# Kernel tuning notes

Hardware: AMD Instinct MI355X
Metric: run time of the kernel (lower is better)

## Reference

```python
import jax, jax.numpy as jnp
import numpy as np

B, S, H = 16, 512, 768
T, HD = 9, 64  # num_entity_types, head_size
MASK_VAL = 1e12


def setup_inputs() -> dict:
    key = jax.random.key(0)
    k1, k2 = jax.random.split(key)
    hidden_states = jax.random.normal(k1, (B, S, H), dtype=jnp.float32)
    attention_mask = jnp.ones((B, S), dtype=jnp.int32)
    W_dense = jax.random.normal(k2, (H, T * HD * 2), dtype=jnp.float32) * (H ** -0.5)
    b_dense = jnp.zeros((T * HD * 2,), dtype=jnp.float32)
    return {"hidden_states": hidden_states, "attention_mask": attention_mask,
            "W_dense": W_dense, "b_dense": b_dense}


def _rope_rotate(x, cos_pos, sin_pos):
    # x: [B, S, T, HD]; rotate interleaved pairs
    x2 = jnp.stack([-x[..., 1::2], x[..., ::2]], axis=-1).reshape(x.shape)
    return x * cos_pos + x2 * sin_pos


def reference(hidden_states, attention_mask, W_dense, b_dense):
    b, s, _ = hidden_states.shape
    out = hidden_states @ W_dense + b_dense              # [B,S,T*HD*2]
    out = out.reshape(b, s, T, HD, 2)
    qw, kw = out[..., 0], out[..., 1]                    # [B,S,T,HD]

    # sinusoidal RoPE angles
    pos = jnp.arange(s, dtype=jnp.float32)               # [S]
    inv_freq = jnp.power(10000.0, -2.0 * jnp.arange(HD // 2, dtype=jnp.float32) / HD)
    ang = pos[:, None] * inv_freq[None, :]               # [S, HD/2]
    cos_pos = jnp.repeat(jnp.cos(ang), 2, axis=-1)[None, :, None, :]  # [1,S,1,HD]
    sin_pos = jnp.repeat(jnp.sin(ang), 2, axis=-1)[None, :, None, :]

    qw = _rope_rotate(qw, cos_pos, sin_pos)
    kw = _rope_rotate(kw, cos_pos, sin_pos)

    # biaffine scores: [B,T,S,S]
    logits = jnp.einsum('bmtd,bntd->btmn', qw, kw) / (HD ** 0.5)

    am = attention_mask.astype(logits.dtype)
    pad_mask = (am[:, :, None] * am[:, None, :])[:, None, :, :]  # [B,1,S,S]
    logits = logits - (1.0 - pad_mask) * MASK_VAL

    triu = jnp.triu(jnp.ones((s, s), dtype=logits.dtype), k=0)
    logits = logits - (1.0 - triu) * MASK_VAL
    return logits
```

## Files before the change

kernel.cpp:

```cpp
#include <hip/hip_runtime.h>

#define B_  16
#define S_  512
#define H_  768
#define T_  9
#define HD_ 64
#define N1  (T_*HD_*2)
#define M1  (B_*S_)
#define NT1 (H_/32)

typedef __attribute__((ext_vector_type(8))) short bf16x8;
typedef __attribute__((ext_vector_type(4))) float f32x4;

#define GLB(p) ((const __attribute__((address_space(1))) void*)(p))
#define LDSP(p) ((__attribute__((address_space(3))) void*)(p))

__device__ inline unsigned short f2bf(float f){
  union { float f; unsigned u; } v; v.f = f;
  unsigned r = v.u + 0x7fffu + ((v.u >> 16) & 1u);
  return (unsigned short)(r >> 16);
}

__global__ __launch_bounds__(256) void prep_all(
    const float* __restrict__ hs, short* __restrict__ Abf,
    const float* __restrict__ W, short* __restrict__ Wt,
    float2* __restrict__ tab)
{
  __shared__ float tile[32][33];
  const int bx = blockIdx.x, tid = threadIdx.x;
  if(bx < 3072){
    int i = bx*2048 + tid*8;
    float4 a0 = *(const float4*)(hs + i);
    float4 a1 = *(const float4*)(hs + i + 4);
    bf16x8 r;
    r[0]=f2bf(a0.x); r[1]=f2bf(a0.y); r[2]=f2bf(a0.z); r[3]=f2bf(a0.w);
    r[4]=f2bf(a1.x); r[5]=f2bf(a1.y); r[6]=f2bf(a1.z); r[7]=f2bf(a1.w);
    *(bf16x8*)(Abf + i) = r;
  } else if(bx < 3936){
    int idx = bx - 3072;
    int n0 = (idx % 36)*32, k0 = (idx / 36)*32;
    int tx = tid & 31, ty = tid >> 5;
    #pragma unroll
    for(int r = 0; r < 32; r += 8)
      tile[ty + r][tx] = W[(size_t)(k0 + ty + r)*N1 + n0 + tx];
    __syncthreads();
    #pragma unroll
    for(int r = 0; r < 32; r += 8)
      Wt[(size_t)(n0 + ty + r)*H_ + k0 + tx] = (short)f2bf(tile[tx][ty + r]);
  } else {
    int i = (bx - 3936)*256 + tid;
    int s = i >> 5, p = i & 31;
    float inv = powf(10000.f, -2.f*(float)p/64.f);
    float a = (float)s * inv;
    tab[i] = make_float2(cosf(a), sinf(a));
  }
}

__global__ __launch_bounds__(256, 3) void gemm1_rope(
    const short* __restrict__ Abf, const short* __restrict__ Wt,
    const float* __restrict__ bias, const float2* __restrict__ tab,
    short* __restrict__ Qr, short* __restrict__ Kr)
{
  __shared__ short As[3][4096];
  __shared__ short Bs[3][4096];
  const int tid  = threadIdx.x;
  const int lane = tid & 63, w = tid >> 6;
  const int lr = lane & 15, h = lane >> 4;
  const int lk = h * 8;
  const int wm = (w >> 1) * 64, wn = (w & 1) * 64;
  const int m0 = blockIdx.x * 128;
  const int n0 = blockIdx.y * 128;

  const short* aS = Abf + (size_t)(m0 + (tid >> 2)) * H_ + (tid & 3) * 8;
  const short* bS = Wt  + (size_t)(n0 + (tid >> 2)) * H_ + (tid & 3) * 8;
  const int dOff = tid * 8;

#define STAGE(buf, k0) do{ \
    __builtin_amdgcn_global_load_lds(GLB(aS + (k0)),         LDSP(&As[buf][dOff]),        16, 0, 0); \
    __builtin_amdgcn_global_load_lds(GLB(aS + 64*H_ + (k0)), LDSP(&As[buf][dOff + 2048]), 16, 0, 0); \
    __builtin_amdgcn_global_load_lds(GLB(bS + (k0)),         LDSP(&Bs[buf][dOff]),        16, 0, 0); \
    __builtin_amdgcn_global_load_lds(GLB(bS + 64*H_ + (k0)), LDSP(&Bs[buf][dOff + 2048]), 16, 0, 0); \
  }while(0)

  f32x4 acc[4][4] = {};

  STAGE(0, 0);
  STAGE(1, 32);
  asm volatile("s_waitcnt vmcnt(4)\n\ts_barrier" ::: "memory");

  int cur = 0;
  for(int it = 0; it < NT1; ++it){
    if(it + 2 < NT1){
      const int nb = (cur + 2 >= 3) ? cur - 1 : cur + 2;
      STAGE(nb, (it + 2) * 32);
    }

    bf16x8 aF[4], bF[4];
    #pragma unroll
    for(int i = 0; i < 4; ++i) aF[i] = *(const bf16x8*)(&As[cur][(wm + i*16 + lr)*32 + lk]);
    #pragma unroll
    for(int j = 0; j < 4; ++j) bF[j] = *(const bf16x8*)(&Bs[cur][(wn + j*16 + lr)*32 + lk]);
    #pragma unroll
    for(int i = 0; i < 4; ++i)
      #pragma unroll
      for(int j = 0; j < 4; ++j)
        acc[i][j] = __builtin_amdgcn_mfma_f32_16x16x32_bf16(bF[j], aF[i], acc[i][j], 0, 0, 0);

    if(it + 3 < NT1)       asm volatile("s_waitcnt vmcnt(4)\n\ts_barrier" ::: "memory");
    else if(it + 2 < NT1)  asm volatile("s_waitcnt vmcnt(4)\n\ts_barrier" ::: "memory");
    else if(it + 1 < NT1)  asm volatile("s_waitcnt vmcnt(0)\n\ts_barrier" ::: "memory");
    cur = (cur + 1 >= 3) ? 0 : cur + 1;
  }

  const int t = blockIdx.y;
  #pragma unroll
  for(int i = 0; i < 4; ++i){
    int m  = m0 + wm + i*16 + lr;
    int bi = m >> 9, sp = m & 511;
    size_t rowoff = ((size_t)(bi*T_ + t)*S_ + sp)*HD_;
    #pragma unroll
    for(int j = 0; j < 4; ++j){
      int nq  = n0 + wn + j*16 + (h << 2);
      int hd0 = (nq >> 1) & 63;
      int p   = (nq >> 2) & 31;
      float4 bv = *(const float4*)(bias + nq);
      float2 cs = tab[sp*32 + p];
      float q0 = acc[i][j][0] + bv.x;
      float k0v= acc[i][j][1] + bv.y;
      float q1 = acc[i][j][2] + bv.z;
      float k1v= acc[i][j][3] + bv.w;
      float rq0 = q0*cs.x - q1*cs.y, rq1 = q1*cs.x + q0*cs.y;
      float rk0 = k0v*cs.x - k1v*cs.y, rk1 = k1v*cs.x + k0v*cs.y;
      unsigned uq = (unsigned)f2bf(rq0) | ((unsigned)f2bf(rq1) << 16);
      unsigned uk = (unsigned)f2bf(rk0) | ((unsigned)f2bf(rk1) << 16);
      *(unsigned*)(Qr + rowoff + hd0) = uq;
      *(unsigned*)(Kr + rowoff + hd0) = uk;
    }
  }
#undef STAGE
}

__global__ __launch_bounds__(256) void gemm2_mask(
    const short* __restrict__ Qr, const short* __restrict__ Kr,
    const int* __restrict__ am, float* __restrict__ out)
{
  const int lane = threadIdx.x & 63;
  const int w    = threadIdx.x >> 6;
  const int wg   = ((blockIdx.x & 7) * 288) + (blockIdx.x >> 3);
  const int bt   = wg >> 4;
  const int tile = wg & 15;
  const int mt   = tile >> 2, nt = tile & 3;
  const int b    = bt / T_;
  const int n0   = nt * 128 + (w & 1) * 64;
  const int m0   = mt * 128 + (w >> 1) * 64;
  const int lr   = lane & 15;
  const int lk   = (lane >> 4) * 8;
  const int* amb = am + b * S_;

  if(mt > nt){
    #pragma unroll
    for(int i = 0; i < 4; ++i){
      int m = m0 + i*16 + lr;
      float amm = (float)amb[m];
      float* orow = out + ((size_t)bt*S_ + m)*S_;
      #pragma unroll
      for(int j = 0; j < 4; ++j){
        int nq = n0 + j*16 + ((lane >> 4) << 2);
        int4 a4 = *(const int4*)(amb + nq);
        float4 r;
        r.x = -(1.f - amm*(float)a4.x)*1e12f - 1e12f;
        r.y = -(1.f - amm*(float)a4.y)*1e12f - 1e12f;
        r.z = -(1.f - amm*(float)a4.z)*1e12f - 1e12f;
        r.w = -(1.f - amm*(float)a4.w)*1e12f - 1e12f;
        *(float4*)(orow + nq) = r;
      }
    }
    return;
  }

  const short* Q = Qr + (size_t)bt * S_ * HD_;
  const short* K = Kr + (size_t)bt * S_ * HD_;
  f32x4 acc[4][4] = {};

  #pragma unroll
  for(int ks = 0; ks < HD_; ks += 32){
    bf16x8 aF[4], bF[4];
    #pragma unroll
    for(int i = 0; i < 4; ++i) aF[i] = *(const bf16x8*)(Q + (size_t)(m0 + i*16 + lr)*HD_ + ks + lk);
    #pragma unroll
    for(int j = 0; j < 4; ++j) bF[j] = *(const bf16x8*)(K + (size_t)(n0 + j*16 + lr)*HD_ + ks + lk);
    #pragma unroll
    for(int i = 0; i < 4; ++i)
      #pragma unroll
      for(int j = 0; j < 4; ++j)
        acc[i][j] = __builtin_amdgcn_mfma_f32_16x16x32_bf16(bF[j], aF[i], acc[i][j], 0, 0, 0);
  }

  const bool diag = (mt == nt);
  #pragma unroll
  for(int i = 0; i < 4; ++i){
    int m = m0 + i*16 + lr;
    float amm = (float)amb[m];
    float* orow = out + ((size_t)bt*S_ + m)*S_;
    #pragma unroll
    for(int j = 0; j < 4; ++j){
      int nq = n0 + j*16 + ((lane >> 4) << 2);
      int4 a4 = *(const int4*)(amb + nq);
      float4 r;
      r.x = acc[i][j][0]*0.125f - (1.f - amm*(float)a4.x)*1e12f;
      r.y = acc[i][j][1]*0.125f - (1.f - amm*(float)a4.y)*1e12f;
      r.z = acc[i][j][2]*0.125f - (1.f - amm*(float)a4.z)*1e12f;
      r.w = acc[i][j][3]*0.125f - (1.f - amm*(float)a4.w)*1e12f;
      if(diag){
        if((nq+0) < m) r.x -= 1e12f;
        if((nq+1) < m) r.y -= 1e12f;
        if((nq+2) < m) r.z -= 1e12f;
        if((nq+3) < m) r.w -= 1e12f;
      }
      *(float4*)(orow + nq) = r;
    }
  }
}

extern "C" void kernel_launch(void* const* d_in, const int* in_sizes, int n_in,
                              void* d_out, int out_size, void* d_ws, size_t ws_size,
                              hipStream_t stream)
{
  const float* hs    = (const float*)d_in[0];
  const int*   amask = (const int*)  d_in[1];
  const float* W     = (const float*)d_in[2];
  const float* bias  = (const float*)d_in[3];
  float* out = (float*)d_out;

  char* ws = (char*)d_ws;
  short*  Wt  = (short*) (ws);
  float2* tab = (float2*)(ws + 1769472);
  short*  Qr  = (short*) (ws + 1900544);
  short*  Kr  = (short*) (ws + 11337728);
  short*  Abf = (short*) (ws + 20774912);

  prep_all  <<<4000, 256, 0, stream>>>(hs, Abf, W, Wt, tab);
  gemm1_rope<<<dim3(M1/128, N1/128), 256, 0, stream>>>(Abf, Wt, bias, tab, Qr, Kr);
  gemm2_mask<<<2304, 256, 0, stream>>>(Qr, Kr, amask, out);
}
```

Baseline: 84.16 us.

## Fuse fp32-to-bf16 activation conversion into GEMM1 loader and use nontemporal output stores

```diff
diff --git a/kernel.cpp b/kernel.cpp
--- a/kernel.cpp
+++ b/kernel.cpp
@@ -21,24 +21,18 @@
   return (unsigned short)(r >> 16);
 }
 
-__global__ __launch_bounds__(256) void prep_all(
-    const float* __restrict__ hs, short* __restrict__ Abf,
-    const float* __restrict__ W, short* __restrict__ Wt,
-    float2* __restrict__ tab)
+__device__ inline void nt_store4(float* p, float x, float y, float z, float wv){
+  f32x4 t = {x, y, z, wv};
+  __builtin_nontemporal_store(t, (f32x4*)p);
+}
+
+__global__ __launch_bounds__(256) void prep_wt(
+    const float* __restrict__ W, short* __restrict__ Wt, float2* __restrict__ tab)
 {
   __shared__ float tile[32][33];
   const int bx = blockIdx.x, tid = threadIdx.x;
-  if(bx < 3072){
-    int i = bx*2048 + tid*8;
-    float4 a0 = *(const float4*)(hs + i);
-    float4 a1 = *(const float4*)(hs + i + 4);
-    bf16x8 r;
-    r[0]=f2bf(a0.x); r[1]=f2bf(a0.y); r[2]=f2bf(a0.z); r[3]=f2bf(a0.w);
-    r[4]=f2bf(a1.x); r[5]=f2bf(a1.y); r[6]=f2bf(a1.z); r[7]=f2bf(a1.w);
-    *(bf16x8*)(Abf + i) = r;
-  } else if(bx < 3936){
-    int idx = bx - 3072;
-    int n0 = (idx % 36)*32, k0 = (idx / 36)*32;
+  if(bx < 864){
+    int n0 = (bx % 36)*32, k0 = (bx / 36)*32;
     int tx = tid & 31, ty = tid >> 5;
     #pragma unroll
     for(int r = 0; r < 32; r += 8)
@@ -48,7 +42,7 @@
     for(int r = 0; r < 32; r += 8)
       Wt[(size_t)(n0 + ty + r)*H_ + k0 + tx] = (short)f2bf(tile[tx][ty + r]);
   } else {
-    int i = (bx - 3936)*256 + tid;
+    int i = (bx - 864)*256 + tid;
     int s = i >> 5, p = i & 31;
     float inv = powf(10000.f, -2.f*(float)p/64.f);
     float a = (float)s * inv;
@@ -57,7 +51,7 @@
 }
 
 __global__ __launch_bounds__(256, 3) void gemm1_rope(
-    const short* __restrict__ Abf, const short* __restrict__ Wt,
+    const float* __restrict__ hs, const short* __restrict__ Wt,
     const float* __restrict__ bias, const float2* __restrict__ tab,
     short* __restrict__ Qr, short* __restrict__ Kr)
 {
@@ -71,45 +65,69 @@
   const int m0 = blockIdx.x * 128;
   const int n0 = blockIdx.y * 128;
 
-  const short* aS = Abf + (size_t)(m0 + (tid >> 2)) * H_ + (tid & 3) * 8;
-  const short* bS = Wt  + (size_t)(n0 + (tid >> 2)) * H_ + (tid & 3) * 8;
+  const float* aS = hs + (size_t)(m0 + (tid >> 2)) * H_ + (tid & 3) * 8;
+  const short* bS = Wt + (size_t)(n0 + (tid >> 2)) * H_ + (tid & 3) * 8;
   const int dOff = tid * 8;
 
-#define STAGE(buf, k0) do{ \
-    __builtin_amdgcn_global_load_lds(GLB(aS + (k0)),         LDSP(&As[buf][dOff]),        16, 0, 0); \
-    __builtin_amdgcn_global_load_lds(GLB(aS + 64*H_ + (k0)), LDSP(&As[buf][dOff + 2048]), 16, 0, 0); \
+  float4 rA0, rA1, rA2, rA3;
+  float4 rB0, rB1, rB2, rB3;
+
+#define LOAD_A(RA0,RA1,RA2,RA3, k0) do{ \
+    RA0 = *(const float4*)(aS + (k0));            RA1 = *(const float4*)(aS + (k0) + 4); \
+    RA2 = *(const float4*)(aS + 64*H_ + (k0));    RA3 = *(const float4*)(aS + 64*H_ + (k0) + 4); \
+  }while(0)
+
+#define CVT_DSWRITE(buf, RA0,RA1,RA2,RA3) do{ \
+    bf16x8 t0_, t1_; \
+    t0_[0]=f2bf(RA0.x); t0_[1]=f2bf(RA0.y); t0_[2]=f2bf(RA0.z); t0_[3]=f2bf(RA0.w); \
+    t0_[4]=f2bf(RA1.x); t0_[5]=f2bf(RA1.y); t0_[6]=f2bf(RA1.z); t0_[7]=f2bf(RA1.w); \
+    t1_[0]=f2bf(RA2.x); t1_[1]=f2bf(RA2.y); t1_[2]=f2bf(RA2.z); t1_[3]=f2bf(RA2.w); \
+    t1_[4]=f2bf(RA3.x); t1_[5]=f2bf(RA3.y); t1_[6]=f2bf(RA3.z); t1_[7]=f2bf(RA3.w); \
+    *(bf16x8*)(&As[buf][dOff]) = t0_; \
+    *(bf16x8*)(&As[buf][dOff + 2048]) = t1_; \
+  }while(0)
+
+#define STAGE_B(buf, k0) do{ \
     __builtin_amdgcn_global_load_lds(GLB(bS + (k0)),         LDSP(&Bs[buf][dOff]),        16, 0, 0); \
     __builtin_amdgcn_global_load_lds(GLB(bS + 64*H_ + (k0)), LDSP(&Bs[buf][dOff + 2048]), 16, 0, 0); \
   }while(0)
 
   f32x4 acc[4][4] = {};
 
-  STAGE(0, 0);
-  STAGE(1, 32);
-  asm volatile("s_waitcnt vmcnt(4)\n\ts_barrier" ::: "memory");
-
-  int cur = 0;
-  for(int it = 0; it < NT1; ++it){
-    if(it + 2 < NT1){
-      const int nb = (cur + 2 >= 3) ? cur - 1 : cur + 2;
-      STAGE(nb, (it + 2) * 32);
+  LOAD_A(rA0,rA1,rA2,rA3, 0);
+  CVT_DSWRITE(0, rA0,rA1,rA2,rA3);
+  STAGE_B(0, 0);
+  LOAD_A(rB0,rB1,rB2,rB3, 32);
+  STAGE_B(1, 64);
+  LOAD_A(rA0,rA1,rA2,rA3, 64);
+  asm volatile("s_waitcnt vmcnt(6) lgkmcnt(0)\n\ts_barrier" ::: "memory");
+
+  #pragma unroll
+  for(int k = 0; k < NT1; ++k){
+    const int cb = k % 3;
+    if(k + 1 < NT1){
+      if((k + 1) & 1) CVT_DSWRITE((k+1)%3, rB0,rB1,rB2,rB3);
+      else            CVT_DSWRITE((k+1)%3, rA0,rA1,rA2,rA3);
+    }
+    if(k + 2 < NT1) STAGE_B((k+2)%3, (k + 2) * 32);
+    if(k + 3 < NT1){
+      if((k + 3) & 1) { LOAD_A(rB0,rB1,rB2,rB3, (k + 3) * 32); }
+      else            { LOAD_A(rA0,rA1,rA2,rA3, (k + 3) * 32); }
     }
 
     bf16x8 aF[4], bF[4];
     #pragma unroll
-    for(int i = 0; i < 4; ++i) aF[i] = *(const bf16x8*)(&As[cur][(wm + i*16 + lr)*32 + lk]);
-    #pragma unroll
-    for(int j = 0; j < 4; ++j) bF[j] = *(const bf16x8*)(&Bs[cur][(wn + j*16 + lr)*32 + lk]);
+    for(int i = 0; i < 4; ++i) aF[i] = *(const bf16x8*)(&As[cb][(wm + i*16 + lr)*32 + lk]);
+    #pragma unroll
+    for(int j = 0; j < 4; ++j) bF[j] = *(const bf16x8*)(&Bs[cb][(wn + j*16 + lr)*32 + lk]);
     #pragma unroll
     for(int i = 0; i < 4; ++i)
       #pragma unroll
       for(int j = 0; j < 4; ++j)
         acc[i][j] = __builtin_amdgcn_mfma_f32_16x16x32_bf16(bF[j], aF[i], acc[i][j], 0, 0, 0);
 
-    if(it + 3 < NT1)       asm volatile("s_waitcnt vmcnt(4)\n\ts_barrier" ::: "memory");
-    else if(it + 2 < NT1)  asm volatile("s_waitcnt vmcnt(4)\n\ts_barrier" ::: "memory");
-    else if(it + 1 < NT1)  asm volatile("s_waitcnt vmcnt(0)\n\ts_barrier" ::: "memory");
-    cur = (cur + 1 >= 3) ? 0 : cur + 1;
+    if(k + 2 < NT1)      asm volatile("s_waitcnt vmcnt(6) lgkmcnt(0)\n\ts_barrier" ::: "memory");
+    else if(k + 1 < NT1) asm volatile("s_waitcnt vmcnt(0) lgkmcnt(0)\n\ts_barrier" ::: "memory");
   }
 
   const int t = blockIdx.y;
@@ -137,7 +155,9 @@
       *(unsigned*)(Kr + rowoff + hd0) = uk;
     }
   }
-#undef STAGE
+#undef LOAD_A
+#undef CVT_DSWRITE
+#undef STAGE_B
 }
 
 __global__ __launch_bounds__(256) void gemm2_mask(
@@ -167,12 +187,11 @@
       for(int j = 0; j < 4; ++j){
         int nq = n0 + j*16 + ((lane >> 4) << 2);
         int4 a4 = *(const int4*)(amb + nq);
-        float4 r;
-        r.x = -(1.f - amm*(float)a4.x)*1e12f - 1e12f;
-        r.y = -(1.f - amm*(float)a4.y)*1e12f - 1e12f;
-        r.z = -(1.f - amm*(float)a4.z)*1e12f - 1e12f;
-        r.w = -(1.f - amm*(float)a4.w)*1e12f - 1e12f;
-        *(float4*)(orow + nq) = r;
+        nt_store4(orow + nq,
+                  -(1.f - amm*(float)a4.x)*1e12f - 1e12f,
+                  -(1.f - amm*(float)a4.y)*1e12f - 1e12f,
+                  -(1.f - amm*(float)a4.z)*1e12f - 1e12f,
+                  -(1.f - amm*(float)a4.w)*1e12f - 1e12f);
       }
     }
     return;
@@ -206,18 +225,17 @@
     for(int j = 0; j < 4; ++j){
       int nq = n0 + j*16 + ((lane >> 4) << 2);
       int4 a4 = *(const int4*)(amb + nq);
-      float4 r;
-      r.x = acc[i][j][0]*0.125f - (1.f - amm*(float)a4.x)*1e12f;
-      r.y = acc[i][j][1]*0.125f - (1.f - amm*(float)a4.y)*1e12f;
-      r.z = acc[i][j][2]*0.125f - (1.f - amm*(float)a4.z)*1e12f;
-      r.w = acc[i][j][3]*0.125f - (1.f - amm*(float)a4.w)*1e12f;
+      float rx = acc[i][j][0]*0.125f - (1.f - amm*(float)a4.x)*1e12f;
+      float ry = acc[i][j][1]*0.125f - (1.f - amm*(float)a4.y)*1e12f;
+      float rz = acc[i][j][2]*0.125f - (1.f - amm*(float)a4.z)*1e12f;
+      float rw = acc[i][j][3]*0.125f - (1.f - amm*(float)a4.w)*1e12f;
       if(diag){
-        if((nq+0) < m) r.x -= 1e12f;
-        if((nq+1) < m) r.y -= 1e12f;
-        if((nq+2) < m) r.z -= 1e12f;
-        if((nq+3) < m) r.w -= 1e12f;
+        if((nq+0) < m) rx -= 1e12f;
+        if((nq+1) < m) ry -= 1e12f;
+        if((nq+2) < m) rz -= 1e12f;
+        if((nq+3) < m) rw -= 1e12f;
       }
-      *(float4*)(orow + nq) = r;
+      nt_store4(orow + nq, rx, ry, rz, rw);
     }
   }
 }
@@ -237,9 +255,8 @@
   float2* tab = (float2*)(ws + 1769472);
   short*  Qr  = (short*) (ws + 1900544);
   short*  Kr  = (short*) (ws + 11337728);
-  short*  Abf = (short*) (ws + 20774912);
-
-  prep_all  <<<4000, 256, 0, stream>>>(hs, Abf, W, Wt, tab);
-  gemm1_rope<<<dim3(M1/128, N1/128), 256, 0, stream>>>(Abf, Wt, bias, tab, Qr, Kr);
+
+  prep_wt   <<<928, 256, 0, stream>>>(W, Wt, tab);
+  gemm1_rope<<<dim3(M1/128, N1/128), 256, 0, stream>>>(hs, Wt, bias, tab, Qr, Kr);
   gemm2_mask<<<2304, 256, 0, stream>>>(Qr, Kr, amask, out);
 }
```

New measurement: 96.13 us. 14.2% more time.
